# Optimization experiments

Hardware: AMD Instinct MI355X
Metric: run time of the kernel (lower is better)

## Reference

```python
import jax, jax.numpy as jnp
import numpy as np

SCALE = 1.0 / np.sqrt(1024.0).astype(np.float32)


def setup_inputs() -> dict:
    key = jax.random.key(0)
    k1, k2, k3, k4, k5, k6 = jax.random.split(key, 6)
    B, Lq, Lk, D_in, D = 8, 2048, 2048, 1024, 256
    data1 = jax.random.normal(k1, (B, Lq, D_in), dtype=jnp.float32)
    data2 = jax.random.normal(k2, (B, Lk, D), dtype=jnp.float32)
    Wq = jax.random.normal(k3, (D_in, D), dtype=jnp.float32) * (1.0 / np.sqrt(D_in))
    bq = jax.random.normal(k4, (D,), dtype=jnp.float32) * 0.01
    Wk = jax.random.normal(k5, (D, D), dtype=jnp.float32) * (1.0 / np.sqrt(D))
    bk = jax.random.normal(k6, (D,), dtype=jnp.float32) * 0.01
    return {"data1": data1, "data2": data2, "Wq": Wq, "bq": bq, "Wk": Wk, "bk": bk}


def reference(data1, data2, Wq, bq, Wk, bk):
    # query: [B, Lq, D], key: [B, Lk, D]
    query = jnp.einsum('bli,id->bld', data1, Wq) + bq
    key = jnp.einsum('bli,id->bld', data2, Wk) + bk
    # scores: [B, Lq, Lk], scaled by sqrt(1024) as in the original
    scores = jnp.einsum('bqd,bkd->bqk', query, key) * SCALE
    attn = jax.nn.softmax(scores, axis=-1)
    # key reused as value; fused residual add with query
    context = jnp.einsum('bqk,bkd->bqd', attn, key) + query
    return context
```

## Files before the change

kernel.cpp:

```cpp
#include <hip/hip_runtime.h>
#include <hip/hip_bf16.h>

typedef __bf16 bf16x8 __attribute__((ext_vector_type(8)));
typedef __bf16 bf16x2 __attribute__((ext_vector_type(2)));
typedef unsigned short u16x8 __attribute__((ext_vector_type(8)));
typedef float f32x4 __attribute__((ext_vector_type(4)));
typedef float f32x16 __attribute__((ext_vector_type(16)));

#define MFMA(a, b, c) __builtin_amdgcn_mfma_f32_16x16x32_bf16(a, b, c, 0, 0, 0)
#define MFMA32(a, b, c) __builtin_amdgcn_mfma_f32_32x32x16_bf16(a, b, c, 0, 0, 0)

#define LQ 2048
#define DD 256

static __device__ __forceinline__ float bf2f(unsigned short u) {
  union { unsigned int i; float f; } x; x.i = ((unsigned int)u) << 16; return x.f;
}
static __device__ __forceinline__ unsigned short f2bf(float f) {
  union { float f; unsigned int i; } x; x.f = f;
  unsigned int r = x.i + 0x7fffu + ((x.i >> 16) & 1u);
  return (unsigned short)(r >> 16);
}
static __device__ __forceinline__ void gll16(const void* g, void* l) {
  __builtin_amdgcn_global_load_lds(
      (const __attribute__((address_space(1))) unsigned int*)g,
      (__attribute__((address_space(3))) unsigned int*)l, 16, 0, 0);
}
static __device__ __forceinline__ unsigned pack2(float a, float b) {
  union { bf16x2 v; unsigned u; } x;
  x.v[0] = (__bf16)a; x.v[1] = (__bf16)b;
  return x.u;
}

__global__ void wt2_kernel(const float* __restrict__ Wq, unsigned short* __restrict__ WqT,
                           const float* __restrict__ Wk, unsigned short* __restrict__ WkT) {
  int id = blockIdx.x * 256 + threadIdx.x;
  if (id < 262144) {
    int n = id >> 10, k = id & 1023;
    WqT[id] = f2bf(Wq[k * 256 + n]);
  } else {
    int j = id - 262144;
    int n = j >> 8, k = j & 255;
    WkT[j] = f2bf(Wk[k * 256 + n]);
  }
}

__global__ __launch_bounds__(256) void proj_kernel(
    const float* __restrict__ A, const unsigned short* __restrict__ WT,
    const float* __restrict__ bias, unsigned short* __restrict__ outb,
    unsigned short* __restrict__ outT, int Kd) {
  __shared__ unsigned short A_s[64 * 32];
  __shared__ unsigned short B_s[128 * 32];
  const int tid = threadIdx.x;
  const int w = tid >> 6, lane = tid & 63, g = lane >> 4, c = lane & 15;
  const int m0 = (blockIdx.x >> 1) * 64, n0 = (blockIdx.x & 1) * 128;
  const int wr = (w >> 1) * 32, wc = (w & 1) * 64;

  f32x4 acc[2][4];
  const f32x4 z4 = {0.f, 0.f, 0.f, 0.f};
  for (int i = 0; i < 2; i++)
    for (int j = 0; j < 4; j++) acc[i][j] = z4;

  const int row_a = tid >> 2, k0a = (tid & 3) * 8;
  const int row_b = tid >> 1, k0b = (tid & 1) * 16;
  const unsigned swz_a = (unsigned)((row_a & 7) << 4);
  const unsigned swz_b = (unsigned)((row_b & 7) << 4);
  const int nk = Kd >> 5;
  for (int ks = 0; ks < nk; ks++) {
    {
      const float* src = A + (long)(m0 + row_a) * Kd + ks * 32 + k0a;
      f32x4 a0 = *(const f32x4*)(src);
      f32x4 a1 = *(const f32x4*)(src + 4);
      bf16x8 t0;
#pragma unroll
      for (int j = 0; j < 4; j++) { t0[j] = (__bf16)a0[j]; t0[4 + j] = (__bf16)a1[j]; }
      *(bf16x8*)((char*)A_s + (((unsigned)(row_a * 64 + k0a * 2)) ^ swz_a)) = t0;
      const unsigned short* srcB = WT + (long)(n0 + row_b) * Kd + ks * 32 + k0b;
      u16x8 b0 = *(const u16x8*)srcB;
      u16x8 b1 = *(const u16x8*)(srcB + 8);
      *(u16x8*)((char*)B_s + (((unsigned)(row_b * 64 + k0b * 2)) ^ swz_b)) = b0;
      *(u16x8*)((char*)B_s + (((unsigned)(row_b * 64 + k0b * 2 + 16)) ^ swz_b)) = b1;
    }
    __syncthreads();
    bf16x8 af[2], bfr[4];
    for (int rf = 0; rf < 2; rf++) {
      int row = wr + rf * 16 + c;
      af[rf] = *(const bf16x8*)((char*)A_s +
                (((unsigned)(row * 64 + g * 16)) ^ ((row & 7) << 4)));
    }
    for (int cf = 0; cf < 4; cf++) {
      int row = wc + cf * 16 + c;
      bfr[cf] = *(const bf16x8*)((char*)B_s +
                (((unsigned)(row * 64 + g * 16)) ^ ((row & 7) << 4)));
    }
    for (int rf = 0; rf < 2; rf++)
      for (int cf = 0; cf < 4; cf++)
        acc[rf][cf] = MFMA(af[rf], bfr[cf], acc[rf][cf]);
    __syncthreads();
  }
  for (int cf = 0; cf < 4; cf++) {
    const int col = n0 + wc + cf * 16 + c;
    const float bv = bias[col];
    for (int rf = 0; rf < 2; rf++) {
      const int row0 = m0 + wr + rf * 16 + g * 4;
      unsigned short pk[4];
      for (int i = 0; i < 4; i++) {
        float v = acc[rf][cf][i] + bv;
        pk[i] = f2bf(v);
        outb[(long)(row0 + i) * 256 + col] = pk[i];
      }
      if (outT) {
        const int b = row0 >> 11;
        const int key0 = row0 & 2047;
        unsigned long long packed = (unsigned long long)pk[0] |
                                    ((unsigned long long)pk[1] << 16) |
                                    ((unsigned long long)pk[2] << 32) |
                                    ((unsigned long long)pk[3] << 48);
        *(unsigned long long*)(outT + ((long)(b * 256 + col) * LQ + key0)) = packed;
      }
    }
  }
}

template <int NSPLIT>
__global__ __launch_bounds__(256, 2) void attn_kernel(
    const unsigned short* __restrict__ Qb, const unsigned short* __restrict__ Kb,
    const unsigned short* __restrict__ KTb, unsigned short* __restrict__ Op,
    float* __restrict__ out, float* __restrict__ ML) {
  constexpr int KS = 2048 / NSPLIT;
  constexpr int NT = KS / 32;
  constexpr int NBLK = 128 * NSPLIT;
  __shared__ char Ks[2][16384];
  __shared__ char KTs[2][16384];
  const int tid = threadIdx.x;
  const int w = tid >> 6, lane = tid & 63;
  const int l5 = lane >> 5, q31 = lane & 31;
  const int lid = (blockIdx.x & 7) * (NBLK / 8) + (blockIdx.x >> 3);
  const int ksplit = lid & (NSPLIT - 1), qg = lid / NSPLIT;
  const int b = qg >> 4;
  const long qrow0 = (long)qg * 128;
  const int kbase = ksplit * KS;
  const float CS = 0.03125f * 1.4426950408889634f;
  const float THRM = 8.0f / CS;

  bf16x8 qf[16];
  {
    const unsigned short* qp = Qb + (qrow0 + w * 32 + q31) * DD + l5 * 8;
#pragma unroll
    for (int s = 0; s < 16; s++) qf[s] = *(const bf16x8*)(qp + s * 16);
  }
  f32x16 o[8];
#pragma unroll
  for (int t = 0; t < 8; t++) o[t] = (f32x16)(0.f);
  float m_ = -1e30f, l_ = 0.f;

  const char* kb_b = (const char*)(Kb + (long)b * LQ * DD);
  const char* kt_b = (const char*)(KTb + (long)b * DD * LQ);

#define STAGE(buf, kt_)                                                          \
  {                                                                              \
    const int k0_ = kbase + (kt_) * 32;                                          \
    const char* kbp_ = kb_b + (long)(k0_ + q31) * 512 + l5 * 16;                 \
    _Pragma("unroll") for (int i = 0; i < 4; i++) {                              \
      const int sl = w * 4 + i;                                                  \
      gll16(kbp_ + sl * 32, Ks[buf] + sl * 1024);                                \
    }                                                                            \
    _Pragma("unroll") for (int i = 0; i < 4; i++) {                              \
      const int th = w * 4 + i;                                                  \
      gll16(kt_b + (long)((th >> 1) * 32 + q31) * 4096 + (long)k0_ * 2 +         \
                (th & 1) * 32 + l5 * 16,                                         \
            KTs[buf] + th * 1024);                                               \
    }                                                                            \
  }

  STAGE(0, 0);
  for (int kt = 0; kt < NT; kt++) {
    const int cur = kt & 1;
    __syncthreads();
    if (kt + 1 < NT) STAGE(cur ^ 1, kt + 1);

    const char* kr = Ks[cur] + lane * 16;
    f32x16 s = (f32x16)(0.f);
#pragma unroll
    for (int sl = 0; sl < 16; sl++) {
      bf16x8 kf = *(const bf16x8*)(kr + sl * 1024);
      s = MFMA32(kf, qf[sl], s);
    }

    float mx = s[0];
#pragma unroll
    for (int r = 1; r < 16; r++) mx = fmaxf(mx, s[r]);
    mx = fmaxf(mx, __shfl_xor(mx, 32));
    if (__any(mx > m_ + THRM)) {
      float mn = fmaxf(m_, mx);
      float al = exp2f((m_ - mn) * CS);
      m_ = mn;
      l_ *= al;
#pragma unroll
      for (int t = 0; t < 8; t++) o[t] *= al;
    }
    const float mCS = m_ * CS;
    float p[16];
    float ls = 0.f;
#pragma unroll
    for (int r = 0; r < 16; r++) {
      p[r] = exp2f(s[r] * CS - mCS);
      ls += p[r];
    }
    l_ += ls;

    unsigned pk[8];
#pragma unroll
    for (int j = 0; j < 8; j++) pk[j] = pack2(p[2 * j], p[2 * j + 1]);
    unsigned x0 = (unsigned)__shfl_xor((int)pk[0], 32);
    unsigned x1 = (unsigned)__shfl_xor((int)pk[1], 32);
    unsigned x2 = (unsigned)__shfl_xor((int)pk[2], 32);
    unsigned x3 = (unsigned)__shfl_xor((int)pk[3], 32);
    unsigned x4 = (unsigned)__shfl_xor((int)pk[4], 32);
    unsigned x5 = (unsigned)__shfl_xor((int)pk[5], 32);
    unsigned x6 = (unsigned)__shfl_xor((int)pk[6], 32);
    unsigned x7 = (unsigned)__shfl_xor((int)pk[7], 32);
    union { unsigned u[4]; bf16x8 v; } pf0, pf1;
    const bool hi = (l5 != 0);
    pf0.u[0] = hi ? x2 : pk[0];
    pf0.u[1] = hi ? x3 : pk[1];
    pf0.u[2] = hi ? pk[2] : x0;
    pf0.u[3] = hi ? pk[3] : x1;
    pf1.u[0] = hi ? x6 : pk[4];
    pf1.u[1] = hi ? x7 : pk[5];
    pf1.u[2] = hi ? pk[6] : x4;
    pf1.u[3] = hi ? pk[7] : x5;

    const char* vr = KTs[cur] + lane * 16;
#pragma unroll
    for (int t = 0; t < 8; t++) {
      bf16x8 v0 = *(const bf16x8*)(vr + (t * 2) * 1024);
      bf16x8 v1 = *(const bf16x8*)(vr + (t * 2 + 1) * 1024);
      o[t] = MFMA32(v0, pf0.v, o[t]);
      o[t] = MFMA32(v1, pf1.v, o[t]);
    }
  }
#undef STAGE

  l_ += __shfl_xor(l_, 32);

  const long orow = (qrow0 + w * 32 + q31) * (long)DD;
  if (ksplit == NSPLIT - 1) {
    float* op = out + orow;
#pragma unroll
    for (int t = 0; t < 8; t++)
#pragma unroll
      for (int r = 0; r < 16; r++)
        op[t * 32 + (r & 3) + 8 * (r >> 2) + 4 * l5] = o[t][r];
  } else {
    unsigned short* opb = Op + (long)ksplit * (16384 * 256) + orow;
#pragma unroll
    for (int t = 0; t < 8; t++)
#pragma unroll
      for (int r = 0; r < 16; r++)
        opb[t * 32 + (r & 3) + 8 * (r >> 2) + 4 * l5] = f2bf(o[t][r]);
  }
  if (lane < 32) {
    float* mlp = ML + (long)(qg * NSPLIT + ksplit) * 256;
    mlp[w * 32 + q31] = m_;
    mlp[128 + w * 32 + q31] = l_;
  }
}

template <int NSPLIT>
__global__ __launch_bounds__(256) void merge_kernel(
    const unsigned short* __restrict__ Op, const float* __restrict__ ML,
    const unsigned short* __restrict__ Qb, float* __restrict__ out) {
  const float CS = 0.03125f * 1.4426950408889634f;
  const long gid = (long)blockIdx.x * 256 + threadIdx.x;
  const long idx = gid * 8;
  const int row = (int)(idx >> 8);
  const int qg = row >> 7, qr = row & 127;
  const float* mlb = ML + (long)(qg * NSPLIT) * 256;
  float mv[NSPLIT], lv[NSPLIT];
#pragma unroll
  for (int k = 0; k < NSPLIT; k++) {
    mv[k] = mlb[k * 256 + qr];
    lv[k] = mlb[k * 256 + 128 + qr];
  }
  float M = mv[0];
#pragma unroll
  for (int k = 1; k < NSPLIT; k++) M = fmaxf(M, mv[k]);
  float ek[NSPLIT], wsum = 0.f;
#pragma unroll
  for (int k = 0; k < NSPLIT; k++) {
    ek[k] = exp2f((mv[k] - M) * CS);
    wsum += ek[k] * lv[k];
  }
  const float inv = 1.0f / wsum;
  float acc[8];
  {
    f32x4 pa = *(const f32x4*)(out + idx);
    f32x4 pb = *(const f32x4*)(out + idx + 4);
#pragma unroll
    for (int e = 0; e < 4; e++) {
      acc[e] = ek[NSPLIT - 1] * pa[e];
      acc[4 + e] = ek[NSPLIT - 1] * pb[e];
    }
  }
#pragma unroll
  for (int k = 0; k < NSPLIT - 1; k++) {
    u16x8 p = *(const u16x8*)(Op + (long)k * (16384 * 256) + idx);
#pragma unroll
    for (int e = 0; e < 8; e++) acc[e] += ek[k] * bf2f(p[e]);
  }
  u16x8 qv = *(const u16x8*)(Qb + idx);
  f32x4 ra, rb;
#pragma unroll
  for (int e = 0; e < 4; e++) ra[e] = acc[e] * inv + bf2f(qv[e]);
#pragma unroll
  for (int e = 0; e < 4; e++) rb[e] = acc[4 + e] * inv + bf2f(qv[4 + e]);
  *(f32x4*)(out + idx) = ra;
  *(f32x4*)(out + idx + 4) = rb;
}

extern "C" void kernel_launch(void* const* d_in, const int* in_sizes, int n_in,
                              void* d_out, int out_size, void* d_ws, size_t ws_size,
                              hipStream_t stream) {
  (void)in_sizes; (void)n_in; (void)out_size;
  const float* data1 = (const float*)d_in[0];
  const float* data2 = (const float*)d_in[1];
  const float* Wq = (const float*)d_in[2];
  const float* bq = (const float*)d_in[3];
  const float* Wk = (const float*)d_in[4];
  const float* bk = (const float*)d_in[5];
  float* out = (float*)d_out;

  char* ws = (char*)d_ws;
  unsigned short* Qb  = (unsigned short*)(ws);
  unsigned short* Kb  = (unsigned short*)(ws + (8ull << 20));
  unsigned short* KTb = (unsigned short*)(ws + (16ull << 20));
  unsigned short* WqT = (unsigned short*)(ws + (24ull << 20));
  unsigned short* WkT = (unsigned short*)(ws + (24ull << 20) + (512u << 10));
  unsigned short* Op  = (unsigned short*)(ws + (25ull << 20));

  wt2_kernel<<<dim3(1280), dim3(256), 0, stream>>>(Wq, WqT, Wk, WkT);
  proj_kernel<<<dim3(512), dim3(256), 0, stream>>>(data1, WqT, bq, Qb,
                                                   (unsigned short*)nullptr, 1024);
  proj_kernel<<<dim3(512), dim3(256), 0, stream>>>(data2, WkT, bk, Kb, KTb, 256);

  if (ws_size >= (50ull << 20)) {
    float* MLb = (float*)(ws + (49ull << 20));
    attn_kernel<4><<<dim3(512), dim3(256), 0, stream>>>(Qb, Kb, KTb, Op, out, MLb);
    merge_kernel<4><<<dim3(2048), dim3(256), 0, stream>>>(Op, MLb, Qb, out);
  } else {
    float* MLb = (float*)(ws + (33ull << 20));
    attn_kernel<2><<<dim3(256), dim3(256), 0, stream>>>(Qb, Kb, KTb, Op, out, MLb);
    merge_kernel<2><<<dim3(2048), dim3(256), 0, stream>>>(Op, MLb, Qb, out);
  }
}
```

Measured before the change: 113.1 us.

## Widen projection tile to full 256 columns with 512-thread blocks

New measurement: 127.3 us. +12.6%, slower.

```diff
diff --git a/kernel.cpp b/kernel.cpp
--- a/kernel.cpp
+++ b/kernel.cpp
@@ -4,6 +4,7 @@
 typedef __bf16 bf16x8 __attribute__((ext_vector_type(8)));
 typedef __bf16 bf16x2 __attribute__((ext_vector_type(2)));
 typedef unsigned short u16x8 __attribute__((ext_vector_type(8)));
+typedef unsigned short u16x4 __attribute__((ext_vector_type(4)));
 typedef float f32x4 __attribute__((ext_vector_type(4)));
 typedef float f32x16 __attribute__((ext_vector_type(16)));
 
@@ -45,23 +46,23 @@
   }
 }
 
-__global__ __launch_bounds__(256) void proj_kernel(
+__global__ __launch_bounds__(512) void proj_kernel(
     const float* __restrict__ A, const unsigned short* __restrict__ WT,
     const float* __restrict__ bias, unsigned short* __restrict__ outb,
     unsigned short* __restrict__ outT, int Kd) {
   __shared__ unsigned short A_s[64 * 32];
-  __shared__ unsigned short B_s[128 * 32];
+  __shared__ unsigned short B_s[256 * 32];
   const int tid = threadIdx.x;
   const int w = tid >> 6, lane = tid & 63, g = lane >> 4, c = lane & 15;
-  const int m0 = (blockIdx.x >> 1) * 64, n0 = (blockIdx.x & 1) * 128;
-  const int wr = (w >> 1) * 32, wc = (w & 1) * 64;
-
-  f32x4 acc[2][4];
+  const int m0 = blockIdx.x * 64;
+  const int wr = (w >> 1) * 16, wc = (w & 1) * 128;
+
+  f32x4 acc[8];
   const f32x4 z4 = {0.f, 0.f, 0.f, 0.f};
-  for (int i = 0; i < 2; i++)
-    for (int j = 0; j < 4; j++) acc[i][j] = z4;
-
-  const int row_a = tid >> 2, k0a = (tid & 3) * 8;
+#pragma unroll
+  for (int j = 0; j < 8; j++) acc[j] = z4;
+
+  const int row_a = tid >> 3, k0a = (tid & 7) * 4;
   const int row_b = tid >> 1, k0b = (tid & 1) * 16;
   const unsigned swz_a = (unsigned)((row_a & 7) << 4);
   const unsigned swz_b = (unsigned)((row_b & 7) << 4);
@@ -70,54 +71,56 @@
     {
       const float* src = A + (long)(m0 + row_a) * Kd + ks * 32 + k0a;
       f32x4 a0 = *(const f32x4*)(src);
-      f32x4 a1 = *(const f32x4*)(src + 4);
-      bf16x8 t0;
-#pragma unroll
-      for (int j = 0; j < 4; j++) { t0[j] = (__bf16)a0[j]; t0[4 + j] = (__bf16)a1[j]; }
-      *(bf16x8*)((char*)A_s + (((unsigned)(row_a * 64 + k0a * 2)) ^ swz_a)) = t0;
-      const unsigned short* srcB = WT + (long)(n0 + row_b) * Kd + ks * 32 + k0b;
+      u16x4 t0;
+#pragma unroll
+      for (int j = 0; j < 4; j++) {
+        union { __bf16 b; unsigned short u; } cv; cv.b = (__bf16)a0[j]; t0[j] = cv.u;
+      }
+      *(u16x4*)((char*)A_s + (((unsigned)(row_a * 64 + k0a * 2)) ^ swz_a)) = t0;
+      const unsigned short* srcB = WT + (long)row_b * Kd + ks * 32 + k0b;
       u16x8 b0 = *(const u16x8*)srcB;
       u16x8 b1 = *(const u16x8*)(srcB + 8);
       *(u16x8*)((char*)B_s + (((unsigned)(row_b * 64 + k0b * 2)) ^ swz_b)) = b0;
       *(u16x8*)((char*)B_s + (((unsigned)(row_b * 64 + k0b * 2 + 16)) ^ swz_b)) = b1;
     }
     __syncthreads();
-    bf16x8 af[2], bfr[4];
-    for (int rf = 0; rf < 2; rf++) {
-      int row = wr + rf * 16 + c;
-      af[rf] = *(const bf16x8*)((char*)A_s +
-                (((unsigned)(row * 64 + g * 16)) ^ ((row & 7) << 4)));
-    }
-    for (int cf = 0; cf < 4; cf++) {
+    bf16x8 af, bfr[8];
+    {
+      int row = wr + c;
+      af = *(const bf16x8*)((char*)A_s +
+            (((unsigned)(row * 64 + g * 16)) ^ ((row & 7) << 4)));
+    }
+#pragma unroll
+    for (int cf = 0; cf < 8; cf++) {
       int row = wc + cf * 16 + c;
       bfr[cf] = *(const bf16x8*)((char*)B_s +
                 (((unsigned)(row * 64 + g * 16)) ^ ((row & 7) << 4)));
     }
-    for (int rf = 0; rf < 2; rf++)
-      for (int cf = 0; cf < 4; cf++)
-        acc[rf][cf] = MFMA(af[rf], bfr[cf], acc[rf][cf]);
+#pragma unroll
+    for (int cf = 0; cf < 8; cf++)
+      acc[cf] = MFMA(af, bfr[cf], acc[cf]);
     __syncthreads();
   }
-  for (int cf = 0; cf < 4; cf++) {
-    const int col = n0 + wc + cf * 16 + c;
+  const int row0 = m0 + wr + g * 4;
+#pragma unroll
+  for (int cf = 0; cf < 8; cf++) {
+    const int col = wc + cf * 16 + c;
     const float bv = bias[col];
-    for (int rf = 0; rf < 2; rf++) {
-      const int row0 = m0 + wr + rf * 16 + g * 4;
-      unsigned short pk[4];
-      for (int i = 0; i < 4; i++) {
-        float v = acc[rf][cf][i] + bv;
-        pk[i] = f2bf(v);
-        outb[(long)(row0 + i) * 256 + col] = pk[i];
-      }
-      if (outT) {
-        const int b = row0 >> 11;
-        const int key0 = row0 & 2047;
-        unsigned long long packed = (unsigned long long)pk[0] |
-                                    ((unsigned long long)pk[1] << 16) |
-                                    ((unsigned long long)pk[2] << 32) |
-                                    ((unsigned long long)pk[3] << 48);
-        *(unsigned long long*)(outT + ((long)(b * 256 + col) * LQ + key0)) = packed;
-      }
+    unsigned short pk[4];
+#pragma unroll
+    for (int i = 0; i < 4; i++) {
+      float v = acc[cf][i] + bv;
+      pk[i] = f2bf(v);
+      outb[(long)(row0 + i) * 256 + col] = pk[i];
+    }
+    if (outT) {
+      const int b = row0 >> 11;
+      const int key0 = row0 & 2047;
+      unsigned long long packed = (unsigned long long)pk[0] |
+                                  ((unsigned long long)pk[1] << 16) |
+                                  ((unsigned long long)pk[2] << 32) |
+                                  ((unsigned long long)pk[3] << 48);
+      *(unsigned long long*)(outT + ((long)(b * 256 + col) * LQ + key0)) = packed;
     }
   }
 }
@@ -340,9 +343,9 @@
   unsigned short* Op  = (unsigned short*)(ws + (25ull << 20));
 
   wt2_kernel<<<dim3(1280), dim3(256), 0, stream>>>(Wq, WqT, Wk, WkT);
-  proj_kernel<<<dim3(512), dim3(256), 0, stream>>>(data1, WqT, bq, Qb,
+  proj_kernel<<<dim3(256), dim3(512), 0, stream>>>(data1, WqT, bq, Qb,
                                                    (unsigned short*)nullptr, 1024);
-  proj_kernel<<<dim3(512), dim3(256), 0, stream>>>(data2, WkT, bk, Kb, KTb, 256);
+  proj_kernel<<<dim3(256), dim3(512), 0, stream>>>(data2, WkT, bk, Kb, KTb, 256);
 
   if (ws_size >= (50ull << 20)) {
     float* MLb = (float*)(ws + (49ull << 20));
```

## Double-buffer projection GEMM with async LDS loads for weights and register prefetch

Applied to the files above, without the earlier changes.

Measured after the change: 110.4 us. 1.02x faster.

```diff
diff --git a/kernel.cpp b/kernel.cpp
--- a/kernel.cpp
+++ b/kernel.cpp
@@ -4,6 +4,7 @@
 typedef __bf16 bf16x8 __attribute__((ext_vector_type(8)));
 typedef __bf16 bf16x2 __attribute__((ext_vector_type(2)));
 typedef unsigned short u16x8 __attribute__((ext_vector_type(8)));
+typedef unsigned short u16x4 __attribute__((ext_vector_type(4)));
 typedef float f32x4 __attribute__((ext_vector_type(4)));
 typedef float f32x16 __attribute__((ext_vector_type(16)));
 
@@ -49,8 +50,8 @@
     const float* __restrict__ A, const unsigned short* __restrict__ WT,
     const float* __restrict__ bias, unsigned short* __restrict__ outb,
     unsigned short* __restrict__ outT, int Kd) {
-  __shared__ unsigned short A_s[64 * 32];
-  __shared__ unsigned short B_s[128 * 32];
+  __shared__ unsigned short A_s[2][64 * 32];
+  __shared__ unsigned short B_s[2][128 * 32];
   const int tid = threadIdx.x;
   const int w = tid >> 6, lane = tid & 63, g = lane >> 4, c = lane & 15;
   const int m0 = (blockIdx.x >> 1) * 64, n0 = (blockIdx.x & 1) * 128;
@@ -58,52 +59,94 @@
 
   f32x4 acc[2][4];
   const f32x4 z4 = {0.f, 0.f, 0.f, 0.f};
+#pragma unroll
   for (int i = 0; i < 2; i++)
+#pragma unroll
     for (int j = 0; j < 4; j++) acc[i][j] = z4;
 
   const int row_a = tid >> 2, k0a = (tid & 3) * 8;
-  const int row_b = tid >> 1, k0b = (tid & 1) * 16;
   const unsigned swz_a = (unsigned)((row_a & 7) << 4);
-  const unsigned swz_b = (unsigned)((row_b & 7) << 4);
+  const float* asrc = A + (long)(m0 + row_a) * Kd + k0a;
+  const int brow0 = w * 32 + (lane >> 2);
+
+#define GLLB(buf, ks_)                                                         \
+  _Pragma("unroll") for (int j = 0; j < 2; j++) {                              \
+    const int brow = brow0 + j * 16;                                           \
+    gll16((const char*)WT + (long)(n0 + brow) * (long)(Kd * 2) + (ks_) * 64 +  \
+              (((lane & 3) * 16) ^ ((brow & 3) << 4)),                         \
+          (char*)B_s[buf] + w * 2048 + j * 1024);                              \
+  }
+
+#define WRA(buf, plo, phi)                                                     \
+  {                                                                            \
+    bf16x8 t;                                                                  \
+    _Pragma("unroll") for (int jj = 0; jj < 4; jj++) {                         \
+      t[jj] = (__bf16)(plo)[jj]; t[4 + jj] = (__bf16)(phi)[jj];                \
+    }                                                                          \
+    *(bf16x8*)((char*)A_s[buf] +                                               \
+               (((unsigned)(row_a * 64 + k0a * 2)) ^ swz_a)) = t;              \
+  }
+
+#define COMPUTE(buf)                                                           \
+  {                                                                            \
+    bf16x8 af[2], bfr[4];                                                      \
+    _Pragma("unroll") for (int rf = 0; rf < 2; rf++) {                         \
+      const int row = wr + rf * 16 + c;                                        \
+      af[rf] = *(const bf16x8*)((char*)A_s[buf] +                              \
+               (((unsigned)(row * 64 + g * 16)) ^ ((row & 7) << 4)));          \
+    }                                                                          \
+    _Pragma("unroll") for (int cf = 0; cf < 4; cf++) {                         \
+      const int row = wc + cf * 16 + c;                                        \
+      bfr[cf] = *(const bf16x8*)((char*)B_s[buf] + row * 64 +                  \
+               (((unsigned)(g * 16)) ^ ((unsigned)((row & 3) << 4))));         \
+    }                                                                          \
+    _Pragma("unroll") for (int rf = 0; rf < 2; rf++)                           \
+      _Pragma("unroll") for (int cf = 0; cf < 4; cf++)                         \
+        acc[rf][cf] = MFMA(af[rf], bfr[cf], acc[rf][cf]);                      \
+  }
+
   const int nk = Kd >> 5;
-  for (int ks = 0; ks < nk; ks++) {
-    {
-      const float* src = A + (long)(m0 + row_a) * Kd + ks * 32 + k0a;
-      f32x4 a0 = *(const f32x4*)(src);
-      f32x4 a1 = *(const f32x4*)(src + 4);
-      bf16x8 t0;
-#pragma unroll
-      for (int j = 0; j < 4; j++) { t0[j] = (__bf16)a0[j]; t0[4 + j] = (__bf16)a1[j]; }
-      *(bf16x8*)((char*)A_s + (((unsigned)(row_a * 64 + k0a * 2)) ^ swz_a)) = t0;
-      const unsigned short* srcB = WT + (long)(n0 + row_b) * Kd + ks * 32 + k0b;
-      u16x8 b0 = *(const u16x8*)srcB;
-      u16x8 b1 = *(const u16x8*)(srcB + 8);
-      *(u16x8*)((char*)B_s + (((unsigned)(row_b * 64 + k0b * 2)) ^ swz_b)) = b0;
-      *(u16x8*)((char*)B_s + (((unsigned)(row_b * 64 + k0b * 2 + 16)) ^ swz_b)) = b1;
-    }
+  f32x4 pe0, pe1, po0, po1;
+  pe0 = *(const f32x4*)(asrc);       pe1 = *(const f32x4*)(asrc + 4);
+  GLLB(0, 0);
+  po0 = *(const f32x4*)(asrc + 32);  po1 = *(const f32x4*)(asrc + 36);
+  WRA(0, pe0, pe1);
+  pe0 = *(const f32x4*)(asrc + 64);  pe1 = *(const f32x4*)(asrc + 68);
+  __syncthreads();
+
+  for (int t = 0; t < nk; t += 2) {
+    GLLB(1, t + 1);
+    WRA(1, po0, po1);
+    if (t + 3 < nk) {
+      po0 = *(const f32x4*)(asrc + (t + 3) * 32);
+      po1 = *(const f32x4*)(asrc + (t + 3) * 32 + 4);
+    }
+    COMPUTE(0);
     __syncthreads();
-    bf16x8 af[2], bfr[4];
-    for (int rf = 0; rf < 2; rf++) {
-      int row = wr + rf * 16 + c;
-      af[rf] = *(const bf16x8*)((char*)A_s +
-                (((unsigned)(row * 64 + g * 16)) ^ ((row & 7) << 4)));
-    }
-    for (int cf = 0; cf < 4; cf++) {
-      int row = wc + cf * 16 + c;
-      bfr[cf] = *(const bf16x8*)((char*)B_s +
-                (((unsigned)(row * 64 + g * 16)) ^ ((row & 7) << 4)));
-    }
-    for (int rf = 0; rf < 2; rf++)
-      for (int cf = 0; cf < 4; cf++)
-        acc[rf][cf] = MFMA(af[rf], bfr[cf], acc[rf][cf]);
+    if (t + 2 < nk) {
+      GLLB(0, t + 2);
+      WRA(0, pe0, pe1);
+      if (t + 4 < nk) {
+        pe0 = *(const f32x4*)(asrc + (t + 4) * 32);
+        pe1 = *(const f32x4*)(asrc + (t + 4) * 32 + 4);
+      }
+    }
+    COMPUTE(1);
     __syncthreads();
   }
+#undef GLLB
+#undef WRA
+#undef COMPUTE
+
+#pragma unroll
   for (int cf = 0; cf < 4; cf++) {
     const int col = n0 + wc + cf * 16 + c;
     const float bv = bias[col];
+#pragma unroll
     for (int rf = 0; rf < 2; rf++) {
       const int row0 = m0 + wr + rf * 16 + g * 4;
       unsigned short pk[4];
+#pragma unroll
       for (int i = 0; i < 4; i++) {
         float v = acc[rf][cf][i] + bv;
         pk[i] = f2bf(v);
```
